# Performance work log

Measured on AMD Instinct MI355X. Metric: run time of the kernel, lower is better.

The kernel has to match this reference:

```python
import jax, jax.numpy as jnp
import numpy as np

EPS = 1e-5
C_M, C, C_Z = 256, 32, 128
N_SEQ, N_RES = 256, 1024


def setup_inputs() -> dict:
    key = jax.random.key(0)
    k1, k2, k3 = jax.random.split(key, 3)
    msa = jax.random.normal(k1, (N_SEQ, N_RES, C_M), dtype=jnp.float32)
    norm_w = jnp.ones((C_M,), dtype=jnp.float32)
    norm_b = jnp.zeros((C_M,), dtype=jnp.float32)
    w_ab = jax.random.normal(k2, (C, C_M), dtype=jnp.float32) * (1.0 / np.sqrt(C_M))
    b_ab = jnp.zeros((C,), dtype=jnp.float32)
    w_out = jax.random.normal(k3, (C_Z, C * C), dtype=jnp.float32) * (1.0 / C)
    b_out = jnp.zeros((C_Z,), dtype=jnp.float32)
    return {"msa": msa, "norm_w": norm_w, "norm_b": norm_b,
            "w_ab": w_ab, "b_ab": b_ab, "w_out": w_out, "b_out": b_out}


def reference(msa, norm_w, norm_b, w_ab, b_ab, w_out, b_out):
    # msa: (s, r, c_m) -> (r, s, c_m)
    x = jnp.transpose(msa, (1, 0, 2))
    s = x.shape[1]
    # LayerNorm over c_m
    mu = jnp.mean(x, axis=-1, keepdims=True)
    var = jnp.mean(jnp.square(x - mu), axis=-1, keepdims=True)
    xn = (x - mu) * jax.lax.rsqrt(var + EPS) * norm_w + norm_b
    # a == b: same linear applied twice to same input in the original
    a = jnp.einsum('rsm,cm->rsc', xn, w_ab) + b_ab          # (r, s, c)
    # mean over s of outer product == batched A^T A / s  -> (r, c, c)
    o = jnp.einsum('rsx,rsy->rxy', a, a) / s
    o = o.reshape(o.shape[0], C * C)                        # (r, c*c)
    pre_pair = jnp.einsum('rk,zk->rz', o, w_out) + b_out    # (r, c_z)
    r = pre_pair.shape[0]
    # unsqueeze(1).expand(r, r, c_z)
    pair = jnp.broadcast_to(pre_pair[:, None, :], (r, r, C_Z))
    return pair
```

## Files before the change

### kernel.cpp

```cpp
#include <hip/hip_runtime.h>

#define NSEQ 256
#define NRES 1024
#define CM   256
#define CC   32
#define CZ   128
#define EPS  1e-5f
#define SROW (NRES * CM)
#define MCH  32
#define XPAD 36

typedef float f4v __attribute__((ext_vector_type(4)));

__launch_bounds__(256, 2)
__global__ void opm_fused(const float* __restrict__ msa,
                          const float* __restrict__ nw,
                          const float* __restrict__ nb,
                          const float* __restrict__ w_ab,
                          const float* __restrict__ b_ab,
                          const float* __restrict__ w_out,
                          const float* __restrict__ b_out,
                          float* __restrict__ out)
{
    __shared__ float wt[CM * CC];
    __shared__ float xt[NSEQ * XPAD];
    __shared__ float o_lds[CC * CC];
    __shared__ float K1p[8 * CC], K2p[8 * CC];
    __shared__ float K1[CC], K2[CC];
    __shared__ float pre_part[2 * CZ];
    __shared__ float pre_lds[CZ];

    const int tid = threadIdx.x;
    const int r   = blockIdx.x;

    {
        const int c  = tid & 31;
        const int m0 = tid >> 5;
        #pragma unroll
        for (int k = 0; k < 32; ++k) {
            const int m = m0 + (k << 3);
            wt[m * CC + c] = nw[m] * w_ab[c * CM + m];
        }
    }
    __syncthreads();
    {
        const int c    = tid & 31;
        const int part = tid >> 5;
        float k1 = 0.f, k2 = 0.f;
        #pragma unroll 8
        for (int i = 0; i < 32; ++i) {
            const int m = part * 32 + i;
            k1 += wt[m * CC + c];
            k2 = fmaf(nb[m], w_ab[c * CM + m], k2);
        }
        K1p[part * CC + c] = k1;
        K2p[part * CC + c] = k2;
    }
    __syncthreads();
    if (tid < CC) {
        float k1 = 0.f, k2 = 0.f;
        #pragma unroll
        for (int p = 0; p < 8; ++p) { k1 += K1p[p * CC + tid]; k2 += K2p[p * CC + tid]; }
        K1[tid] = k1;
        K2[tid] = k2 + b_ab[tid];
    }

    const int sc = tid & 7;
    const int sg = tid >> 3;
    const int c0 = sc * 4;
    const float* xr = msa + (size_t)r * CM;

    float G[8][4];
    float ssum[8], ssq[8];
    #pragma unroll
    for (int j = 0; j < 8; ++j) {
        ssum[j] = 0.f; ssq[j] = 0.f;
        #pragma unroll
        for (int cc = 0; cc < 4; ++cc) G[j][cc] = 0.f;
    }

    float4 pf[8];
    #pragma unroll
    for (int k = 0; k < 8; ++k)
        pf[k] = *(const float4*)(xr + (size_t)(sg + (k << 5)) * SROW + (sc << 2));

    for (int mb = 0; mb < CM; mb += MCH) {
        __syncthreads();
        #pragma unroll
        for (int k = 0; k < 8; ++k)
            *(float4*)&xt[(sg + (k << 5)) * XPAD + (sc << 2)] = pf[k];
        __syncthreads();
        if (mb + MCH < CM) {
            #pragma unroll
            for (int k = 0; k < 8; ++k)
                pf[k] = *(const float4*)(xr + (size_t)(sg + (k << 5)) * SROW + (mb + MCH) + (sc << 2));
        }
        #pragma unroll
        for (int mm = 0; mm < MCH; mm += 4) {
            const float4 w0 = *(const float4*)&wt[(mb + mm + 0) * CC + c0];
            const float4 w1 = *(const float4*)&wt[(mb + mm + 1) * CC + c0];
            const float4 w2 = *(const float4*)&wt[(mb + mm + 2) * CC + c0];
            const float4 w3 = *(const float4*)&wt[(mb + mm + 3) * CC + c0];
            #pragma unroll
            for (int j = 0; j < 8; ++j) {
                const float4 x4 = *(const float4*)&xt[(sg + (j << 5)) * XPAD + mm];
                G[j][0] = fmaf(x4.x, w0.x, fmaf(x4.y, w1.x, fmaf(x4.z, w2.x, fmaf(x4.w, w3.x, G[j][0]))));
                G[j][1] = fmaf(x4.x, w0.y, fmaf(x4.y, w1.y, fmaf(x4.z, w2.y, fmaf(x4.w, w3.y, G[j][1]))));
                G[j][2] = fmaf(x4.x, w0.z, fmaf(x4.y, w1.z, fmaf(x4.z, w2.z, fmaf(x4.w, w3.z, G[j][2]))));
                G[j][3] = fmaf(x4.x, w0.w, fmaf(x4.y, w1.w, fmaf(x4.z, w2.w, fmaf(x4.w, w3.w, G[j][3]))));
                ssum[j] += (x4.x + x4.y) + (x4.z + x4.w);
                ssq[j]  = fmaf(x4.x, x4.x, fmaf(x4.y, x4.y, fmaf(x4.z, x4.z, fmaf(x4.w, x4.w, ssq[j]))));
            }
        }
    }

    float a_reg[8][4];
    {
        const float k1a = K1[c0 + 0], k1b = K1[c0 + 1], k1c = K1[c0 + 2], k1d = K1[c0 + 3];
        const float k2a = K2[c0 + 0], k2b = K2[c0 + 1], k2c = K2[c0 + 2], k2d = K2[c0 + 3];
        #pragma unroll
        for (int j = 0; j < 8; ++j) {
            const float mu   = ssum[j] * (1.f / CM);
            const float var  = ssq[j] * (1.f / CM) - mu * mu;
            const float rstd = 1.f / sqrtf(var + EPS);
            a_reg[j][0] = fmaf(rstd, G[j][0] - mu * k1a, k2a);
            a_reg[j][1] = fmaf(rstd, G[j][1] - mu * k1b, k2b);
            a_reg[j][2] = fmaf(rstd, G[j][2] - mu * k1c, k2c);
            a_reg[j][3] = fmaf(rstd, G[j][3] - mu * k1d, k2d);
        }
    }
    __syncthreads();
    #pragma unroll
    for (int j = 0; j < 8; ++j) {
        const int s = sg + (j << 5);
        *(float4*)&xt[s * CC + c0] =
            make_float4(a_reg[j][0], a_reg[j][1], a_reg[j][2], a_reg[j][3]);
    }
    __syncthreads();

    const int xi = (tid >> 4) << 1;
    const int yi = (tid & 15) << 1;
    float o00 = 0.f, o01 = 0.f, o10 = 0.f, o11 = 0.f;
    #pragma unroll 4
    for (int s = 0; s < NSEQ; ++s) {
        const float2 ax = *(const float2*)&xt[s * CC + xi];
        const float2 ay = *(const float2*)&xt[s * CC + yi];
        o00 = fmaf(ax.x, ay.x, o00);
        o01 = fmaf(ax.x, ay.y, o01);
        o10 = fmaf(ax.y, ay.x, o10);
        o11 = fmaf(ax.y, ay.y, o11);
    }
    {
        const float inv_s = 1.f / NSEQ;
        *(float2*)&o_lds[xi * CC + yi]       = make_float2(o00 * inv_s, o01 * inv_s);
        *(float2*)&o_lds[(xi + 1) * CC + yi] = make_float2(o10 * inv_s, o11 * inv_s);
    }
    __syncthreads();

    {
        const int z    = tid & 127;
        const int half = tid >> 7;
        const float* wrow = w_out + (size_t)z * (CC * CC) + half * 512;
        const float* op   = o_lds + half * 512;
        float po = 0.f;
        #pragma unroll 8
        for (int k = 0; k < 512; k += 4) {
            const float4 o4 = *(const float4*)&op[k];
            const float4 w4 = *(const float4*)&wrow[k];
            po = fmaf(o4.x, w4.x, fmaf(o4.y, w4.y, fmaf(o4.z, w4.z, fmaf(o4.w, w4.w, po))));
        }
        pre_part[half * CZ + z] = po;
    }
    __syncthreads();
    if (tid < CZ) pre_lds[tid] = pre_part[tid] + pre_part[CZ + tid] + b_out[tid];
    __syncthreads();

    {
        const int z4 = tid & 31;
        const int jo = tid >> 5;
        f4v pv;
        pv.x = pre_lds[z4 * 4 + 0];
        pv.y = pre_lds[z4 * 4 + 1];
        pv.z = pre_lds[z4 * 4 + 2];
        pv.w = pre_lds[z4 * 4 + 3];
        f4v* outp = (f4v*)out + (size_t)r * NRES * (CZ / 4);
        for (int j0 = 0; j0 < NRES; j0 += 8) {
            __builtin_nontemporal_store(pv, &outp[(size_t)(j0 + jo) * (CZ / 4) + z4]);
        }
    }
}

extern "C" void kernel_launch(void* const* d_in, const int* in_sizes, int n_in,
                              void* d_out, int out_size, void* d_ws, size_t ws_size,
                              hipStream_t stream) {
    const float* msa   = (const float*)d_in[0];
    const float* nw    = (const float*)d_in[1];
    const float* nb    = (const float*)d_in[2];
    const float* w_ab  = (const float*)d_in[3];
    const float* b_ab  = (const float*)d_in[4];
    const float* w_out = (const float*)d_in[5];
    const float* b_out = (const float*)d_in[6];
    float* out = (float*)d_out;

    opm_fused<<<NRES, 256, 0, stream>>>(msa, nw, nb, w_ab, b_ab, w_out, b_out, out);
}
```

Before: 839.5 us.

## Split broadcast into separate kernel and compute LayerNorm stats from prefetch registers

The fused kernel becomes two launches: a compute kernel that writes the per-residue pre_pair vector to workspace, and a broadcast kernel with 8x as many blocks that writes the 512 MB output with nontemporal stores. LayerNorm sum and sum-of-squares now accumulate from the prefetched float4 registers, each thread covering only its own 4 channels, and are reduced with lane shuffles. This takes redundant statistic arithmetic out of the inner FMA loop. The split is meant to spread the store-bound broadcast over more parallel blocks and shorten the compute kernel, at the cost of a second launch and a small workspace round trip.

```diff
diff --git a/kernel.cpp b/kernel.cpp
--- a/kernel.cpp
+++ b/kernel.cpp
@@ -13,14 +13,14 @@
 typedef float f4v __attribute__((ext_vector_type(4)));
 
 __launch_bounds__(256, 2)
-__global__ void opm_fused(const float* __restrict__ msa,
-                          const float* __restrict__ nw,
-                          const float* __restrict__ nb,
-                          const float* __restrict__ w_ab,
-                          const float* __restrict__ b_ab,
-                          const float* __restrict__ w_out,
-                          const float* __restrict__ b_out,
-                          float* __restrict__ out)
+__global__ void opm_compute(const float* __restrict__ msa,
+                            const float* __restrict__ nw,
+                            const float* __restrict__ nb,
+                            const float* __restrict__ w_ab,
+                            const float* __restrict__ b_ab,
+                            const float* __restrict__ w_out,
+                            const float* __restrict__ b_out,
+                            float* __restrict__ pre_out)
 {
     __shared__ float wt[CM * CC];
     __shared__ float xt[NSEQ * XPAD];
@@ -28,7 +28,6 @@
     __shared__ float K1p[8 * CC], K2p[8 * CC];
     __shared__ float K1[CC], K2[CC];
     __shared__ float pre_part[2 * CZ];
-    __shared__ float pre_lds[CZ];
 
     const int tid = threadIdx.x;
     const int r   = blockIdx.x;
@@ -71,10 +70,10 @@
     const float* xr = msa + (size_t)r * CM;
 
     float G[8][4];
-    float ssum[8], ssq[8];
+    float psum[8], pssq[8];
     #pragma unroll
     for (int j = 0; j < 8; ++j) {
-        ssum[j] = 0.f; ssq[j] = 0.f;
+        psum[j] = 0.f; pssq[j] = 0.f;
         #pragma unroll
         for (int cc = 0; cc < 4; ++cc) G[j][cc] = 0.f;
     }
@@ -87,8 +86,12 @@
     for (int mb = 0; mb < CM; mb += MCH) {
         __syncthreads();
         #pragma unroll
-        for (int k = 0; k < 8; ++k)
+        for (int k = 0; k < 8; ++k) {
             *(float4*)&xt[(sg + (k << 5)) * XPAD + (sc << 2)] = pf[k];
+            psum[k] += (pf[k].x + pf[k].y) + (pf[k].z + pf[k].w);
+            pssq[k]  = fmaf(pf[k].x, pf[k].x, fmaf(pf[k].y, pf[k].y,
+                       fmaf(pf[k].z, pf[k].z, fmaf(pf[k].w, pf[k].w, pssq[k]))));
+        }
         __syncthreads();
         if (mb + MCH < CM) {
             #pragma unroll
@@ -108,10 +111,20 @@
                 G[j][1] = fmaf(x4.x, w0.y, fmaf(x4.y, w1.y, fmaf(x4.z, w2.y, fmaf(x4.w, w3.y, G[j][1]))));
                 G[j][2] = fmaf(x4.x, w0.z, fmaf(x4.y, w1.z, fmaf(x4.z, w2.z, fmaf(x4.w, w3.z, G[j][2]))));
                 G[j][3] = fmaf(x4.x, w0.w, fmaf(x4.y, w1.w, fmaf(x4.z, w2.w, fmaf(x4.w, w3.w, G[j][3]))));
-                ssum[j] += (x4.x + x4.y) + (x4.z + x4.w);
-                ssq[j]  = fmaf(x4.x, x4.x, fmaf(x4.y, x4.y, fmaf(x4.z, x4.z, fmaf(x4.w, x4.w, ssq[j]))));
             }
         }
+    }
+
+    float mu_[8], rstd_[8];
+    #pragma unroll
+    for (int j = 0; j < 8; ++j) {
+        float s1 = psum[j], s2 = pssq[j];
+        s1 += __shfl_xor(s1, 1); s1 += __shfl_xor(s1, 2); s1 += __shfl_xor(s1, 4);
+        s2 += __shfl_xor(s2, 1); s2 += __shfl_xor(s2, 2); s2 += __shfl_xor(s2, 4);
+        const float mu  = s1 * (1.f / CM);
+        const float var = s2 * (1.f / CM) - mu * mu;
+        mu_[j]   = mu;
+        rstd_[j] = 1.f / sqrtf(var + EPS);
     }
 
     float a_reg[8][4];
@@ -120,9 +133,7 @@
         const float k2a = K2[c0 + 0], k2b = K2[c0 + 1], k2c = K2[c0 + 2], k2d = K2[c0 + 3];
         #pragma unroll
         for (int j = 0; j < 8; ++j) {
-            const float mu   = ssum[j] * (1.f / CM);
-            const float var  = ssq[j] * (1.f / CM) - mu * mu;
-            const float rstd = 1.f / sqrtf(var + EPS);
+            const float mu = mu_[j], rstd = rstd_[j];
             a_reg[j][0] = fmaf(rstd, G[j][0] - mu * k1a, k2a);
             a_reg[j][1] = fmaf(rstd, G[j][1] - mu * k1b, k2b);
             a_reg[j][2] = fmaf(rstd, G[j][2] - mu * k1c, k2c);
@@ -172,22 +183,24 @@
         pre_part[half * CZ + z] = po;
     }
     __syncthreads();
-    if (tid < CZ) pre_lds[tid] = pre_part[tid] + pre_part[CZ + tid] + b_out[tid];
-    __syncthreads();
-
-    {
-        const int z4 = tid & 31;
-        const int jo = tid >> 5;
-        f4v pv;
-        pv.x = pre_lds[z4 * 4 + 0];
-        pv.y = pre_lds[z4 * 4 + 1];
-        pv.z = pre_lds[z4 * 4 + 2];
-        pv.w = pre_lds[z4 * 4 + 3];
-        f4v* outp = (f4v*)out + (size_t)r * NRES * (CZ / 4);
-        for (int j0 = 0; j0 < NRES; j0 += 8) {
-            __builtin_nontemporal_store(pv, &outp[(size_t)(j0 + jo) * (CZ / 4) + z4]);
-        }
-    }
+    if (tid < CZ)
+        pre_out[(size_t)r * CZ + tid] = pre_part[tid] + pre_part[CZ + tid] + b_out[tid];
+}
+
+__launch_bounds__(256, 8)
+__global__ void opm_bcast(const float* __restrict__ pre,
+                          float* __restrict__ out)
+{
+    const int bid = blockIdx.x;
+    const int r   = bid >> 3;
+    const int jb  = bid & 7;
+    const int z4  = threadIdx.x & 31;
+    const int jo  = threadIdx.x >> 5;
+
+    const f4v pv = *((const f4v*)(pre + (size_t)r * CZ) + z4);
+    f4v* outp = (f4v*)out + ((size_t)r * NRES + (size_t)jb * 128) * (CZ / 4);
+    for (int j0 = 0; j0 < 128; j0 += 8)
+        __builtin_nontemporal_store(pv, &outp[(size_t)(j0 + jo) * (CZ / 4) + z4]);
 }
 
 extern "C" void kernel_launch(void* const* d_in, const int* in_sizes, int n_in,
@@ -201,6 +214,8 @@
     const float* w_out = (const float*)d_in[5];
     const float* b_out = (const float*)d_in[6];
     float* out = (float*)d_out;
-
-    opm_fused<<<NRES, 256, 0, stream>>>(msa, nw, nb, w_ab, b_ab, w_out, b_out, out);
+    float* pre = (float*)d_ws;
+
+    opm_compute<<<NRES, 256, 0, stream>>>(msa, nw, nb, w_ab, b_ab, w_out, b_out, pre);
+    opm_bcast<<<NRES * 8, 256, 0, stream>>>(pre, out);
 }
```

After: 796.6 us. 1.05x faster.
